# Kernel optimization log

Hardware: AMD Instinct MI355X
Metric: run time of the kernel (lower is better)

Reference implementation:

```python
import jax, jax.numpy as jnp
import numpy as np

B, T, V, E, DH, H, M, W = 64, 50, 32000, 64, 128, 8, 256, 50


def setup_inputs() -> dict:
    key = jax.random.key(0)
    ks = jax.random.split(key, 18)
    sc = 0.02
    return {
        "x": jax.random.randint(ks[0], (B, T), 0, V),
        "tok_emb": jax.random.normal(ks[1], (V, E)) * sc,
        "pos_emb": jax.random.normal(ks[2], (W, E)) * sc,
        "Wq": jax.random.normal(ks[3], (H, E, DH)) * sc,
        "bq": jnp.zeros((H, DH)),
        "Wk": jax.random.normal(ks[4], (H, E, DH)) * sc,
        "bk": jnp.zeros((H, DH)),
        "Wv": jax.random.normal(ks[5], (H, E, DH)) * sc,
        "bv": jnp.zeros((H, DH)),
        "Wo": jax.random.normal(ks[6], (H * DH, E)) * sc,
        "bo": jnp.zeros((E,)),
        "W1": jax.random.normal(ks[7], (E, M)) * sc,
        "b1": jnp.zeros((M,)),
        "W2": jax.random.normal(ks[8], (M, E)) * sc,
        "b2": jnp.zeros((E,)),
        "Wf": jax.random.normal(ks[9], (E, V)) * sc,
        "bf": jnp.zeros((V,)),
    }


def reference(x, tok_emb, pos_emb, Wq, bq, Wk, bk, Wv, bv, Wo, bo, W1, b1, W2, b2, Wf, bf):
    b, t = x.shape
    h = tok_emb[x] + pos_emb[:t]  # [B,T,E]
    # batched per-head QKV projections (original loops over 8 heads)
    Q = jnp.einsum("bte,hed->bhtd", h, Wq) + bq[None, :, None, :]
    K = jnp.einsum("bte,hed->bhtd", h, Wk) + bk[None, :, None, :]
    Vv = jnp.einsum("bte,hed->bhtd", h, Wv) + bv[None, :, None, :]
    scores = jnp.einsum("bhtd,bhsd->bhts", Q, K) / (DH ** 0.5)
    # faithful to original: masked_fill(tril(scores) == 0, -inf)
    scores = jnp.where(jnp.tril(scores) == 0, -jnp.inf, scores)
    attn = jax.nn.softmax(scores, axis=-1)
    o = jnp.einsum("bhts,bhsd->bhtd", attn, Vv)
    o = o.transpose(0, 2, 1, 3).reshape(b, t, H * DH)  # concat heads
    a = o @ Wo + bo
    # NOTE: no residual connections in the original module
    m = jax.nn.gelu(a @ W1 + b1, approximate=False)
    y = m @ W2 + b2
    logits = y @ Wf + bf  # [B,T,V]
    return logits
```

## Files before the change

kernel.cpp:

```cpp
#include <hip/hip_runtime.h>
#include <math.h>

#define T_ 50
#define R_ 3200

using u16 = unsigned short;
typedef __attribute__((ext_vector_type(8))) __bf16 bf16x8;
typedef __attribute__((ext_vector_type(4))) float f32x4;

__device__ __forceinline__ float bf2f(u16 u) {
  union { unsigned int i; float f; } x; x.i = ((unsigned int)u) << 16; return x.f;
}
__device__ __forceinline__ u16 f2bf(float f) {
  union { float f; unsigned int i; } x; x.f = f;
  unsigned int r = x.i + 0x7FFFu + ((x.i >> 16) & 1u);
  return (u16)(r >> 16);
}
__device__ __forceinline__ void split2(float v, u16& hi, u16& lo) {
  hi = f2bf(v);
  lo = f2bf(v - bf2f(hi));
}
__device__ __forceinline__ float gelu_f(float v) {
  return 0.5f * v * (1.0f + erff(v * 0.70710678118654752f));
}

__global__ __launch_bounds__(256) void k_prep(
    const int* __restrict__ x, const float* __restrict__ tok, const float* __restrict__ pos,
    const float* __restrict__ Wq, const float* __restrict__ Wk, const float* __restrict__ Wv,
    const float* __restrict__ bq, const float* __restrict__ bk, const float* __restrict__ bv,
    const float* __restrict__ Wo, const float* __restrict__ W1, const float* __restrict__ W2,
    const float* __restrict__ Wf,
    u16* __restrict__ hH, u16* __restrict__ hL,
    u16* __restrict__ WqkvTh, u16* __restrict__ WqkvTl, float* __restrict__ bqkv,
    u16* __restrict__ WoTh, u16* __restrict__ WoTl,
    u16* __restrict__ W1Th, u16* __restrict__ W1Tl,
    u16* __restrict__ W2Th, u16* __restrict__ W2Tl,
    u16* __restrict__ WfTh, u16* __restrict__ WfTl) {
  __shared__ __align__(16) float tile[64][68];
  int bid = blockIdx.x;
  if (bid < 800) {
    int i = bid * 256 + threadIdx.x;
    int row = i >> 6, e = i & 63;
    int t = row % T_;
    int v = x[row];
    split2(tok[(long)v * 64 + e] + pos[t * 64 + e], hH[i], hL[i]);
    return;
  }
  if (bid < 1964) {
    int i = (bid - 800) * 256 + threadIdx.x;
    const int S0 = 196608, S1 = 3072, S2 = 65536, S3 = 16384;
    if (i < S0) {
      int n = i >> 6, e = i & 63;
      int p = n >> 10, rem = n & 1023;
      int hh_ = rem >> 7, d = rem & 127;
      const float* W = (p == 0) ? Wq : ((p == 1) ? Wk : Wv);
      split2(W[hh_ * 8192 + e * 128 + d], WqkvTh[i], WqkvTl[i]);
      return;
    }
    i -= S0;
    if (i < S1) { int p = i >> 10, rem = i & 1023;
      const float* bb = (p == 0) ? bq : ((p == 1) ? bk : bv);
      bqkv[i] = bb[rem]; return; }
    i -= S1;
    if (i < S2) { int n = i >> 10, k = i & 1023;
      split2(Wo[k * 64 + n], WoTh[i], WoTl[i]); return; }
    i -= S2;
    if (i < S3) { int n = i >> 6, k = i & 63;
      split2(W1[k * 256 + n], W1Th[i], W1Tl[i]); return; }
    i -= S3;
    { int n = i >> 8, k = i & 255;
      split2(W2[k * 64 + n], W2Th[i], W2Tl[i]); }
    return;
  }
  int n0 = (bid - 1964) * 64;
  for (int c = threadIdx.x; c < 1024; c += 256) {
    int k = c >> 4, ch = (c & 15) * 4;
    *(float4*)&tile[k][ch] = *(const float4*)&Wf[(long)k * 32000 + n0 + ch];
  }
  __syncthreads();
  for (int c = threadIdx.x; c < 1024; c += 256) {
    int n = c >> 4, ch = (c & 15) * 4;
    u16 th[4], tl[4];
#pragma unroll
    for (int j = 0; j < 4; ++j) split2(tile[ch + j][n], th[j], tl[j]);
    *(ushort4*)&WfTh[(long)(n0 + n) * 64 + ch] = *(ushort4*)th;
    *(ushort4*)&WfTl[(long)(n0 + n) * 64 + ch] = *(ushort4*)tl;
  }
}

__global__ __launch_bounds__(256) void k_attn(const float* __restrict__ QKV,
                                              u16* __restrict__ Oh,
                                              u16* __restrict__ Ol) {
  __shared__ __align__(16) float Kl[64 * 128];
  __shared__ __align__(16) float Vt[128 * 64];
  __shared__ __align__(16) float Qw[4][512];
  __shared__ __align__(16) float Pw[4][256];
  const int bh = blockIdx.x, b = bh >> 3, hd = bh & 7;
  const int tid = threadIdx.x, lane = tid & 63, wave = tid >> 6;
  const float* base = QKV + (long)b * T_ * 3072 + hd * 128;
  for (int c = tid; c < 64 * 32; c += 256) {
    int s = c >> 5, c4 = c & 31;
    float4 kv = make_float4(0.f, 0.f, 0.f, 0.f), vv = kv;
    if (s < T_) {
      const float* rowp = base + (long)s * 3072;
      kv = *(const float4*)(rowp + 1024 + c4 * 4);
      vv = *(const float4*)(rowp + 2048 + c4 * 4);
    }
    *(float4*)&Kl[s * 128 + ((c4 ^ (s & 31)) << 2)] = kv;
    int d0 = c4 * 4, s4 = s >> 2, sm = s & 3;
    Vt[(d0 + 0) * 64 + ((s4 ^ ((d0 + 0) & 15)) << 2) + sm] = vv.x;
    Vt[(d0 + 1) * 64 + ((s4 ^ ((d0 + 1) & 15)) << 2) + sm] = vv.y;
    Vt[(d0 + 2) * 64 + ((s4 ^ ((d0 + 2) & 15)) << 2) + sm] = vv.z;
    Vt[(d0 + 3) * 64 + ((s4 ^ ((d0 + 3) & 15)) << 2) + sm] = vv.w;
  }
  __syncthreads();
  const float scale = 0.0883883476483184406f;
  for (int g = wave; g < 13; g += 4) {
    const int r0 = g * 4;
#pragma unroll
    for (int it = 0; it < 2; ++it) {
      int cc = lane + it * 64;
      int j = cc >> 5, c4q = cc & 31;
      int rq = r0 + j;
      if (rq < T_)
        *(float4*)&Qw[wave][j * 128 + c4q * 4] =
            *(const float4*)&base[(long)rq * 3072 + c4q * 4];
    }
    asm volatile("s_waitcnt lgkmcnt(0)" ::: "memory");
    float p0 = 0.f, p1 = 0.f, p2 = 0.f, p3 = 0.f;
#pragma unroll 8
    for (int c4 = 0; c4 < 32; ++c4) {
      float4 kv = *(const float4*)&Kl[lane * 128 + ((c4 ^ (lane & 31)) << 2)];
      float4 q0 = *(const float4*)&Qw[wave][c4 * 4];
      float4 q1 = *(const float4*)&Qw[wave][128 + c4 * 4];
      float4 q2 = *(const float4*)&Qw[wave][256 + c4 * 4];
      float4 q3 = *(const float4*)&Qw[wave][384 + c4 * 4];
      p0 = fmaf(q0.x, kv.x, p0); p0 = fmaf(q0.y, kv.y, p0);
      p0 = fmaf(q0.z, kv.z, p0); p0 = fmaf(q0.w, kv.w, p0);
      p1 = fmaf(q1.x, kv.x, p1); p1 = fmaf(q1.y, kv.y, p1);
      p1 = fmaf(q1.z, kv.z, p1); p1 = fmaf(q1.w, kv.w, p1);
      p2 = fmaf(q2.x, kv.x, p2); p2 = fmaf(q2.y, kv.y, p2);
      p2 = fmaf(q2.z, kv.z, p2); p2 = fmaf(q2.w, kv.w, p2);
      p3 = fmaf(q3.x, kv.x, p3); p3 = fmaf(q3.y, kv.y, p3);
      p3 = fmaf(q3.z, kv.z, p3); p3 = fmaf(q3.w, kv.w, p3);
    }
    float ps[4] = {p0, p1, p2, p3};
#pragma unroll
    for (int j = 0; j < 4; ++j) {
      int rq = r0 + j;
      float sc = (rq < T_ && lane <= rq) ? ps[j] * scale : -INFINITY;
      float mx = sc;
      mx = fmaxf(mx, __shfl_xor(mx, 32)); mx = fmaxf(mx, __shfl_xor(mx, 16));
      mx = fmaxf(mx, __shfl_xor(mx, 8));  mx = fmaxf(mx, __shfl_xor(mx, 4));
      mx = fmaxf(mx, __shfl_xor(mx, 2));  mx = fmaxf(mx, __shfl_xor(mx, 1));
      float e = expf(sc - mx);
      float sum = e;
      sum += __shfl_xor(sum, 32); sum += __shfl_xor(sum, 16); sum += __shfl_xor(sum, 8);
      sum += __shfl_xor(sum, 4);  sum += __shfl_xor(sum, 2);  sum += __shfl_xor(sum, 1);
      Pw[wave][j * 64 + lane] = e / sum;
    }
    asm volatile("s_waitcnt lgkmcnt(0)" ::: "memory");
    float oa[4] = {0.f, 0.f, 0.f, 0.f};
    float ob[4] = {0.f, 0.f, 0.f, 0.f};
    for (int s4 = 0; s4 <= g; ++s4) {
      int vc = (s4 ^ (lane & 15)) << 2;
      float4 va = *(const float4*)&Vt[lane * 64 + vc];
      float4 vb = *(const float4*)&Vt[(64 + lane) * 64 + vc];
#pragma unroll
      for (int j = 0; j < 4; ++j) {
        float4 pb = *(const float4*)&Pw[wave][j * 64 + s4 * 4];
        oa[j] = fmaf(pb.x, va.x, oa[j]); oa[j] = fmaf(pb.y, va.y, oa[j]);
        oa[j] = fmaf(pb.z, va.z, oa[j]); oa[j] = fmaf(pb.w, va.w, oa[j]);
        ob[j] = fmaf(pb.x, vb.x, ob[j]); ob[j] = fmaf(pb.y, vb.y, ob[j]);
        ob[j] = fmaf(pb.z, vb.z, ob[j]); ob[j] = fmaf(pb.w, vb.w, ob[j]);
      }
    }
#pragma unroll
    for (int j = 0; j < 4; ++j) {
      int rq = r0 + j;
      if (rq < T_) {
        long orow = ((long)b * T_ + rq) * 1024 + hd * 128;
        u16 hi, lo;
        split2(oa[j], hi, lo); Oh[orow + lane] = hi;      Ol[orow + lane] = lo;
        split2(ob[j], hi, lo); Oh[orow + 64 + lane] = hi; Ol[orow + 64 + lane] = lo;
      }
    }
  }
}

template <int WM, int TN, int KK, int ACT, int OSPLIT, int SWZ>
__global__ __launch_bounds__(WM * 64) void k_gemm(
    const u16* __restrict__ Ah, const u16* __restrict__ Al,
    const u16* __restrict__ Bth, const u16* __restrict__ Btl,
    const float* __restrict__ bias,
    float* __restrict__ C, u16* __restrict__ Ch, u16* __restrict__ Cl,
    int ldc, int gm) {
  int id = blockIdx.x;
  if constexpr (SWZ) {
    int nbk = gridDim.x;
    int q = nbk >> 3, r = nbk & 7;
    int xcd = id & 7, idx = id >> 3;
    id = (xcd < r ? xcd * (q + 1) : r * (q + 1) + (xcd - r) * q) + idx;
  }
  const int mb = id % gm, nb = id / gm;
  const int m0 = mb * (WM * 16), n0 = nb * (TN * 16);
  const int tid = threadIdx.x, lane = tid & 63, wave = tid >> 6;
  const int ln = lane & 15, quad = lane >> 4;
  const int mrow = m0 + wave * 16 + ln;
  const long arow = (long)mrow * KK;
  f32x4 acc[TN];
#pragma unroll
  for (int tn = 0; tn < TN; ++tn)
#pragma unroll
    for (int i = 0; i < 4; ++i) acc[tn][i] = 0.f;
#pragma unroll
  for (int k0 = 0; k0 < KK; k0 += 32) {
    bf16x8 a_h = *(const bf16x8*)&Ah[arow + k0 + quad * 8];
    bf16x8 a_l = *(const bf16x8*)&Al[arow + k0 + quad * 8];
#pragma unroll
    for (int tn = 0; tn < TN; ++tn) {
      const long brow = (long)(n0 + tn * 16 + ln) * KK + k0 + quad * 8;
      bf16x8 b_h = *(const bf16x8*)&Bth[brow];
      bf16x8 b_l = *(const bf16x8*)&Btl[brow];
      acc[tn] = __builtin_amdgcn_mfma_f32_16x16x32_bf16(b_h, a_h, acc[tn], 0, 0, 0);
      acc[tn] = __builtin_amdgcn_mfma_f32_16x16x32_bf16(b_h, a_l, acc[tn], 0, 0, 0);
      acc[tn] = __builtin_amdgcn_mfma_f32_16x16x32_bf16(b_l, a_h, acc[tn], 0, 0, 0);
    }
  }
#pragma unroll
  for (int tn = 0; tn < TN; ++tn) {
    int nc = n0 + tn * 16 + quad * 4;
    float4 bv = *(const float4*)&bias[nc];
    float v0 = acc[tn][0] + bv.x, v1 = acc[tn][1] + bv.y;
    float v2 = acc[tn][2] + bv.z, v3 = acc[tn][3] + bv.w;
    if (ACT) { v0 = gelu_f(v0); v1 = gelu_f(v1); v2 = gelu_f(v2); v3 = gelu_f(v3); }
    long idx2 = (long)mrow * ldc + nc;
    if constexpr (OSPLIT) {
      ushort4 hs, ls;
      split2(v0, hs.x, ls.x); split2(v1, hs.y, ls.y);
      split2(v2, hs.z, ls.z); split2(v3, hs.w, ls.w);
      *(ushort4*)&Ch[idx2] = hs;
      *(ushort4*)&Cl[idx2] = ls;
    } else {
      *(float4*)&C[idx2] = make_float4(v0, v1, v2, v3);
    }
  }
}

__global__ __launch_bounds__(64) void k_mlp(
    const u16* __restrict__ oH, const u16* __restrict__ oL,
    const u16* __restrict__ WoTh, const u16* __restrict__ WoTl, const float* __restrict__ bo,
    const u16* __restrict__ W1Th, const u16* __restrict__ W1Tl, const float* __restrict__ b1,
    const u16* __restrict__ W2Th, const u16* __restrict__ W2Tl, const float* __restrict__ b2,
    u16* __restrict__ yH, u16* __restrict__ yL) {
  __shared__ __align__(16) u16 aLh[16][88], aLl[16][88];
  __shared__ __align__(16) u16 mLh[16][264], mLl[16][264];
  const int lane = threadIdx.x, ln = lane & 15, quad = lane >> 4;
  const int r = blockIdx.x * 16 + ln;
  f32x4 acc1[4];
#pragma unroll
  for (int tn = 0; tn < 4; ++tn)
#pragma unroll
    for (int i = 0; i < 4; ++i) acc1[tn][i] = 0.f;
#pragma unroll 4
  for (int k0 = 0; k0 < 1024; k0 += 32) {
    bf16x8 a_h = *(const bf16x8*)&oH[(long)r * 1024 + k0 + quad * 8];
    bf16x8 a_l = *(const bf16x8*)&oL[(long)r * 1024 + k0 + quad * 8];
#pragma unroll
    for (int tn = 0; tn < 4; ++tn) {
      const int brow = (tn * 16 + ln) * 1024 + k0 + quad * 8;
      bf16x8 b_h = *(const bf16x8*)&WoTh[brow];
      bf16x8 b_l = *(const bf16x8*)&WoTl[brow];
      acc1[tn] = __builtin_amdgcn_mfma_f32_16x16x32_bf16(b_h, a_h, acc1[tn], 0, 0, 0);
      acc1[tn] = __builtin_amdgcn_mfma_f32_16x16x32_bf16(b_h, a_l, acc1[tn], 0, 0, 0);
      acc1[tn] = __builtin_amdgcn_mfma_f32_16x16x32_bf16(b_l, a_h, acc1[tn], 0, 0, 0);
    }
  }
#pragma unroll
  for (int tn = 0; tn < 4; ++tn) {
    int nc = tn * 16 + quad * 4;
    float4 bv = *(const float4*)&bo[nc];
    ushort4 hs, ls;
    split2(acc1[tn][0] + bv.x, hs.x, ls.x); split2(acc1[tn][1] + bv.y, hs.y, ls.y);
    split2(acc1[tn][2] + bv.z, hs.z, ls.z); split2(acc1[tn][3] + bv.w, hs.w, ls.w);
    *(ushort4*)&aLh[ln][nc] = hs;
    *(ushort4*)&aLl[ln][nc] = ls;
  }
  __syncthreads();
  f32x4 acc2[16];
#pragma unroll
  for (int tn = 0; tn < 16; ++tn)
#pragma unroll
    for (int i = 0; i < 4; ++i) acc2[tn][i] = 0.f;
#pragma unroll
  for (int k0 = 0; k0 < 64; k0 += 32) {
    bf16x8 a_h = *(const bf16x8*)&aLh[ln][k0 + quad * 8];
    bf16x8 a_l = *(const bf16x8*)&aLl[ln][k0 + quad * 8];
#pragma unroll
    for (int tn = 0; tn < 16; ++tn) {
      const int brow = (tn * 16 + ln) * 64 + k0 + quad * 8;
      bf16x8 b_h = *(const bf16x8*)&W1Th[brow];
      bf16x8 b_l = *(const bf16x8*)&W1Tl[brow];
      acc2[tn] = __builtin_amdgcn_mfma_f32_16x16x32_bf16(b_h, a_h, acc2[tn], 0, 0, 0);
      acc2[tn] = __builtin_amdgcn_mfma_f32_16x16x32_bf16(b_h, a_l, acc2[tn], 0, 0, 0);
      acc2[tn] = __builtin_amdgcn_mfma_f32_16x16x32_bf16(b_l, a_h, acc2[tn], 0, 0, 0);
    }
  }
#pragma unroll
  for (int tn = 0; tn < 16; ++tn) {
    int nc = tn * 16 + quad * 4;
    float4 bv = *(const float4*)&b1[nc];
    ushort4 hs, ls;
    split2(gelu_f(acc2[tn][0] + bv.x), hs.x, ls.x);
    split2(gelu_f(acc2[tn][1] + bv.y), hs.y, ls.y);
    split2(gelu_f(acc2[tn][2] + bv.z), hs.z, ls.z);
    split2(gelu_f(acc2[tn][3] + bv.w), hs.w, ls.w);
    *(ushort4*)&mLh[ln][nc] = hs;
    *(ushort4*)&mLl[ln][nc] = ls;
  }
  __syncthreads();
  f32x4 acc3[4];
#pragma unroll
  for (int tn = 0; tn < 4; ++tn)
#pragma unroll
    for (int i = 0; i < 4; ++i) acc3[tn][i] = 0.f;
#pragma unroll 2
  for (int k0 = 0; k0 < 256; k0 += 32) {
    bf16x8 a_h = *(const bf16x8*)&mLh[ln][k0 + quad * 8];
    bf16x8 a_l = *(const bf16x8*)&mLl[ln][k0 + quad * 8];
#pragma unroll
    for (int tn = 0; tn < 4; ++tn) {
      const int brow = (tn * 16 + ln) * 256 + k0 + quad * 8;
      bf16x8 b_h = *(const bf16x8*)&W2Th[brow];
      bf16x8 b_l = *(const bf16x8*)&W2Tl[brow];
      acc3[tn] = __builtin_amdgcn_mfma_f32_16x16x32_bf16(b_h, a_h, acc3[tn], 0, 0, 0);
      acc3[tn] = __builtin_amdgcn_mfma_f32_16x16x32_bf16(b_h, a_l, acc3[tn], 0, 0, 0);
      acc3[tn] = __builtin_amdgcn_mfma_f32_16x16x32_bf16(b_l, a_h, acc3[tn], 0, 0, 0);
    }
  }
#pragma unroll
  for (int tn = 0; tn < 4; ++tn) {
    int nc = tn * 16 + quad * 4;
    float4 bv = *(const float4*)&b2[nc];
    ushort4 hs, ls;
    split2(acc3[tn][0] + bv.x, hs.x, ls.x); split2(acc3[tn][1] + bv.y, hs.y, ls.y);
    split2(acc3[tn][2] + bv.z, hs.z, ls.z); split2(acc3[tn][3] + bv.w, hs.w, ls.w);
    *(ushort4*)&yH[(long)r * 64 + nc] = hs;
    *(ushort4*)&yL[(long)r * 64 + nc] = ls;
  }
}

extern "C" void kernel_launch(void* const* d_in, const int* in_sizes, int n_in,
                              void* d_out, int out_size, void* d_ws, size_t ws_size,
                              hipStream_t stream) {
  const int*   x   = (const int*)d_in[0];
  const float* tok = (const float*)d_in[1];
  const float* pos = (const float*)d_in[2];
  const float* Wq  = (const float*)d_in[3];
  const float* bq  = (const float*)d_in[4];
  const float* Wk  = (const float*)d_in[5];
  const float* bk  = (const float*)d_in[6];
  const float* Wv  = (const float*)d_in[7];
  const float* bv  = (const float*)d_in[8];
  const float* Wo  = (const float*)d_in[9];
  const float* bo  = (const float*)d_in[10];
  const float* W1  = (const float*)d_in[11];
  const float* b1  = (const float*)d_in[12];
  const float* W2  = (const float*)d_in[13];
  const float* b2  = (const float*)d_in[14];
  const float* Wf  = (const float*)d_in[15];
  const float* bfv = (const float*)d_in[16];

  char* ws = (char*)d_ws;
  float* QKV    = (float*)(ws + 0);
  u16*   oH     = (u16*)(ws + 39321600);
  u16*   oL     = (u16*)(ws + 45875200);
  u16*   hH     = (u16*)(ws + 52428800);
  u16*   hL     = (u16*)(ws + 52838400);
  u16*   yH     = (u16*)(ws + 53248000);
  u16*   yL     = (u16*)(ws + 53657600);
  u16*   WqkvTh = (u16*)(ws + 54067200);
  u16*   WqkvTl = (u16*)(ws + 54460416);
  float* bqkv   = (float*)(ws + 54853632);
  u16*   WoTh   = (u16*)(ws + 54865920);
  u16*   WoTl   = (u16*)(ws + 54996992);
  u16*   W1Th   = (u16*)(ws + 55128064);
  u16*   W1Tl   = (u16*)(ws + 55160832);
  u16*   W2Th   = (u16*)(ws + 55193600);
  u16*   W2Tl   = (u16*)(ws + 55226368);
  u16*   WfTh   = (u16*)(ws + 55259136);
  u16*   WfTl   = (u16*)(ws + 59355136);
  float* out    = (float*)d_out;

  k_prep<<<dim3(2464), 256, 0, stream>>>(x, tok, pos, Wq, Wk, Wv, bq, bk, bv,
      Wo, W1, W2, Wf, hH, hL, WqkvTh, WqkvTl, bqkv, WoTh, WoTl,
      W1Th, W1Tl, W2Th, W2Tl, WfTh, WfTl);
  k_gemm<4, 8, 64, 0, 0, 0><<<dim3(1200), 256, 0, stream>>>(
      hH, hL, WqkvTh, WqkvTl, bqkv, QKV, nullptr, nullptr, 3072, 50);
  k_attn<<<dim3(512), 256, 0, stream>>>(QKV, oH, oL);
  k_mlp<<<dim3(200), 64, 0, stream>>>(oH, oL, WoTh, WoTl, bo,
      W1Th, W1Tl, b1, W2Th, W2Tl, b2, yH, yL);
  k_gemm<4, 8, 64, 0, 0, 1><<<dim3(12500), 256, 0, stream>>>(
      yH, yL, WfTh, WfTl, bfv, out, nullptr, nullptr, 32000, 50);
}
```

Baseline: 732.9 us.

## Stage B tiles in LDS for GEMM and split fused MLP into GEMM launches

Result: faster. 602.7 us (-17.8%).

```diff
diff --git a/kernel.cpp b/kernel.cpp
--- a/kernel.cpp
+++ b/kernel.cpp
@@ -188,13 +188,18 @@
   }
 }
 
-template <int WM, int TN, int KK, int ACT, int OSPLIT, int SWZ>
-__global__ __launch_bounds__(WM * 64) void k_gemm(
+template <int BN, int BK, int ACT, int OSPLIT, int SWZ>
+__global__ __launch_bounds__(256) void k_gemm(
     const u16* __restrict__ Ah, const u16* __restrict__ Al,
     const u16* __restrict__ Bth, const u16* __restrict__ Btl,
     const float* __restrict__ bias,
     float* __restrict__ C, u16* __restrict__ Ch, u16* __restrict__ Cl,
-    int ldc, int gm) {
+    int ldc, int K, int gm) {
+  constexpr int BM = 64;
+  constexpr int TN = BN / 16;
+  constexpr int BKW = BK / 8;
+  __shared__ __align__(16) u16 Bh[BN][BK + 8];
+  __shared__ __align__(16) u16 Bl[BN][BK + 8];
   int id = blockIdx.x;
   if constexpr (SWZ) {
     int nbk = gridDim.x;
@@ -202,30 +207,40 @@
     int xcd = id & 7, idx = id >> 3;
     id = (xcd < r ? xcd * (q + 1) : r * (q + 1) + (xcd - r) * q) + idx;
   }
-  const int mb = id % gm, nb = id / gm;
-  const int m0 = mb * (WM * 16), n0 = nb * (TN * 16);
+  const int m0 = (id % gm) * BM, n0 = (id / gm) * BN;
   const int tid = threadIdx.x, lane = tid & 63, wave = tid >> 6;
   const int ln = lane & 15, quad = lane >> 4;
   const int mrow = m0 + wave * 16 + ln;
-  const long arow = (long)mrow * KK;
+  const long arow = (long)mrow * K;
   f32x4 acc[TN];
 #pragma unroll
   for (int tn = 0; tn < TN; ++tn)
 #pragma unroll
     for (int i = 0; i < 4; ++i) acc[tn][i] = 0.f;
-#pragma unroll
-  for (int k0 = 0; k0 < KK; k0 += 32) {
-    bf16x8 a_h = *(const bf16x8*)&Ah[arow + k0 + quad * 8];
-    bf16x8 a_l = *(const bf16x8*)&Al[arow + k0 + quad * 8];
-#pragma unroll
-    for (int tn = 0; tn < TN; ++tn) {
-      const long brow = (long)(n0 + tn * 16 + ln) * KK + k0 + quad * 8;
-      bf16x8 b_h = *(const bf16x8*)&Bth[brow];
-      bf16x8 b_l = *(const bf16x8*)&Btl[brow];
-      acc[tn] = __builtin_amdgcn_mfma_f32_16x16x32_bf16(b_h, a_h, acc[tn], 0, 0, 0);
-      acc[tn] = __builtin_amdgcn_mfma_f32_16x16x32_bf16(b_h, a_l, acc[tn], 0, 0, 0);
-      acc[tn] = __builtin_amdgcn_mfma_f32_16x16x32_bf16(b_l, a_h, acc[tn], 0, 0, 0);
-    }
+
+  for (int kk = 0; kk < K; kk += BK) {
+#pragma unroll
+    for (int c0 = 0; c0 < BN * BKW; c0 += 256) {
+      int c = c0 + tid;
+      int rr = c / BKW, c8 = (c % BKW) * 8;
+      *(uint4*)&Bh[rr][c8] = *(const uint4*)&Bth[(long)(n0 + rr) * K + kk + c8];
+      *(uint4*)&Bl[rr][c8] = *(const uint4*)&Btl[(long)(n0 + rr) * K + kk + c8];
+    }
+    __syncthreads();
+#pragma unroll
+    for (int ks = 0; ks < BK / 32; ++ks) {
+      bf16x8 a_h = *(const bf16x8*)&Ah[arow + kk + ks * 32 + quad * 8];
+      bf16x8 a_l = *(const bf16x8*)&Al[arow + kk + ks * 32 + quad * 8];
+#pragma unroll
+      for (int tn = 0; tn < TN; ++tn) {
+        bf16x8 b_h = *(const bf16x8*)&Bh[tn * 16 + ln][ks * 32 + quad * 8];
+        bf16x8 b_l = *(const bf16x8*)&Bl[tn * 16 + ln][ks * 32 + quad * 8];
+        acc[tn] = __builtin_amdgcn_mfma_f32_16x16x32_bf16(b_h, a_h, acc[tn], 0, 0, 0);
+        acc[tn] = __builtin_amdgcn_mfma_f32_16x16x32_bf16(b_h, a_l, acc[tn], 0, 0, 0);
+        acc[tn] = __builtin_amdgcn_mfma_f32_16x16x32_bf16(b_l, a_h, acc[tn], 0, 0, 0);
+      }
+    }
+    __syncthreads();
   }
 #pragma unroll
   for (int tn = 0; tn < TN; ++tn) {
@@ -244,109 +259,6 @@
     } else {
       *(float4*)&C[idx2] = make_float4(v0, v1, v2, v3);
     }
-  }
-}
-
-__global__ __launch_bounds__(64) void k_mlp(
-    const u16* __restrict__ oH, const u16* __restrict__ oL,
-    const u16* __restrict__ WoTh, const u16* __restrict__ WoTl, const float* __restrict__ bo,
-    const u16* __restrict__ W1Th, const u16* __restrict__ W1Tl, const float* __restrict__ b1,
-    const u16* __restrict__ W2Th, const u16* __restrict__ W2Tl, const float* __restrict__ b2,
-    u16* __restrict__ yH, u16* __restrict__ yL) {
-  __shared__ __align__(16) u16 aLh[16][88], aLl[16][88];
-  __shared__ __align__(16) u16 mLh[16][264], mLl[16][264];
-  const int lane = threadIdx.x, ln = lane & 15, quad = lane >> 4;
-  const int r = blockIdx.x * 16 + ln;
-  f32x4 acc1[4];
-#pragma unroll
-  for (int tn = 0; tn < 4; ++tn)
-#pragma unroll
-    for (int i = 0; i < 4; ++i) acc1[tn][i] = 0.f;
-#pragma unroll 4
-  for (int k0 = 0; k0 < 1024; k0 += 32) {
-    bf16x8 a_h = *(const bf16x8*)&oH[(long)r * 1024 + k0 + quad * 8];
-    bf16x8 a_l = *(const bf16x8*)&oL[(long)r * 1024 + k0 + quad * 8];
-#pragma unroll
-    for (int tn = 0; tn < 4; ++tn) {
-      const int brow = (tn * 16 + ln) * 1024 + k0 + quad * 8;
-      bf16x8 b_h = *(const bf16x8*)&WoTh[brow];
-      bf16x8 b_l = *(const bf16x8*)&WoTl[brow];
-      acc1[tn] = __builtin_amdgcn_mfma_f32_16x16x32_bf16(b_h, a_h, acc1[tn], 0, 0, 0);
-      acc1[tn] = __builtin_amdgcn_mfma_f32_16x16x32_bf16(b_h, a_l, acc1[tn], 0, 0, 0);
-      acc1[tn] = __builtin_amdgcn_mfma_f32_16x16x32_bf16(b_l, a_h, acc1[tn], 0, 0, 0);
-    }
-  }
-#pragma unroll
-  for (int tn = 0; tn < 4; ++tn) {
-    int nc = tn * 16 + quad * 4;
-    float4 bv = *(const float4*)&bo[nc];
-    ushort4 hs, ls;
-    split2(acc1[tn][0] + bv.x, hs.x, ls.x); split2(acc1[tn][1] + bv.y, hs.y, ls.y);
-    split2(acc1[tn][2] + bv.z, hs.z, ls.z); split2(acc1[tn][3] + bv.w, hs.w, ls.w);
-    *(ushort4*)&aLh[ln][nc] = hs;
-    *(ushort4*)&aLl[ln][nc] = ls;
-  }
-  __syncthreads();
-  f32x4 acc2[16];
-#pragma unroll
-  for (int tn = 0; tn < 16; ++tn)
-#pragma unroll
-    for (int i = 0; i < 4; ++i) acc2[tn][i] = 0.f;
-#pragma unroll
-  for (int k0 = 0; k0 < 64; k0 += 32) {
-    bf16x8 a_h = *(const bf16x8*)&aLh[ln][k0 + quad * 8];
-    bf16x8 a_l = *(const bf16x8*)&aLl[ln][k0 + quad * 8];
-#pragma unroll
-    for (int tn = 0; tn < 16; ++tn) {
-      const int brow = (tn * 16 + ln) * 64 + k0 + quad * 8;
-      bf16x8 b_h = *(const bf16x8*)&W1Th[brow];
-      bf16x8 b_l = *(const bf16x8*)&W1Tl[brow];
-      acc2[tn] = __builtin_amdgcn_mfma_f32_16x16x32_bf16(b_h, a_h, acc2[tn], 0, 0, 0);
-      acc2[tn] = __builtin_amdgcn_mfma_f32_16x16x32_bf16(b_h, a_l, acc2[tn], 0, 0, 0);
-      acc2[tn] = __builtin_amdgcn_mfma_f32_16x16x32_bf16(b_l, a_h, acc2[tn], 0, 0, 0);
-    }
-  }
-#pragma unroll
-  for (int tn = 0; tn < 16; ++tn) {
-    int nc = tn * 16 + quad * 4;
-    float4 bv = *(const float4*)&b1[nc];
-    ushort4 hs, ls;
-    split2(gelu_f(acc2[tn][0] + bv.x), hs.x, ls.x);
-    split2(gelu_f(acc2[tn][1] + bv.y), hs.y, ls.y);
-    split2(gelu_f(acc2[tn][2] + bv.z), hs.z, ls.z);
-    split2(gelu_f(acc2[tn][3] + bv.w), hs.w, ls.w);
-    *(ushort4*)&mLh[ln][nc] = hs;
-    *(ushort4*)&mLl[ln][nc] = ls;
-  }
-  __syncthreads();
-  f32x4 acc3[4];
-#pragma unroll
-  for (int tn = 0; tn < 4; ++tn)
-#pragma unroll
-    for (int i = 0; i < 4; ++i) acc3[tn][i] = 0.f;
-#pragma unroll 2
-  for (int k0 = 0; k0 < 256; k0 += 32) {
-    bf16x8 a_h = *(const bf16x8*)&mLh[ln][k0 + quad * 8];
-    bf16x8 a_l = *(const bf16x8*)&mLl[ln][k0 + quad * 8];
-#pragma unroll
-    for (int tn = 0; tn < 4; ++tn) {
-      const int brow = (tn * 16 + ln) * 256 + k0 + quad * 8;
-      bf16x8 b_h = *(const bf16x8*)&W2Th[brow];
-      bf16x8 b_l = *(const bf16x8*)&W2Tl[brow];
-      acc3[tn] = __builtin_amdgcn_mfma_f32_16x16x32_bf16(b_h, a_h, acc3[tn], 0, 0, 0);
-      acc3[tn] = __builtin_amdgcn_mfma_f32_16x16x32_bf16(b_h, a_l, acc3[tn], 0, 0, 0);
-      acc3[tn] = __builtin_amdgcn_mfma_f32_16x16x32_bf16(b_l, a_h, acc3[tn], 0, 0, 0);
-    }
-  }
-#pragma unroll
-  for (int tn = 0; tn < 4; ++tn) {
-    int nc = tn * 16 + quad * 4;
-    float4 bv = *(const float4*)&b2[nc];
-    ushort4 hs, ls;
-    split2(acc3[tn][0] + bv.x, hs.x, ls.x); split2(acc3[tn][1] + bv.y, hs.y, ls.y);
-    split2(acc3[tn][2] + bv.z, hs.z, ls.z); split2(acc3[tn][3] + bv.w, hs.w, ls.w);
-    *(ushort4*)&yH[(long)r * 64 + nc] = hs;
-    *(ushort4*)&yL[(long)r * 64 + nc] = ls;
   }
 }
 
@@ -377,29 +289,37 @@
   u16*   oL     = (u16*)(ws + 45875200);
   u16*   hH     = (u16*)(ws + 52428800);
   u16*   hL     = (u16*)(ws + 52838400);
-  u16*   yH     = (u16*)(ws + 53248000);
-  u16*   yL     = (u16*)(ws + 53657600);
-  u16*   WqkvTh = (u16*)(ws + 54067200);
-  u16*   WqkvTl = (u16*)(ws + 54460416);
-  float* bqkv   = (float*)(ws + 54853632);
-  u16*   WoTh   = (u16*)(ws + 54865920);
-  u16*   WoTl   = (u16*)(ws + 54996992);
-  u16*   W1Th   = (u16*)(ws + 55128064);
-  u16*   W1Tl   = (u16*)(ws + 55160832);
-  u16*   W2Th   = (u16*)(ws + 55193600);
-  u16*   W2Tl   = (u16*)(ws + 55226368);
-  u16*   WfTh   = (u16*)(ws + 55259136);
-  u16*   WfTl   = (u16*)(ws + 59355136);
+  u16*   aH     = (u16*)(ws + 53248000);
+  u16*   aL     = (u16*)(ws + 53657600);
+  u16*   mH     = (u16*)(ws + 54067200);
+  u16*   mL     = (u16*)(ws + 55705600);
+  u16*   yH     = (u16*)(ws + 57344000);
+  u16*   yL     = (u16*)(ws + 57753600);
+  u16*   WqkvTh = (u16*)(ws + 58163200);
+  u16*   WqkvTl = (u16*)(ws + 58556416);
+  float* bqkv   = (float*)(ws + 58949632);
+  u16*   WoTh   = (u16*)(ws + 58961920);
+  u16*   WoTl   = (u16*)(ws + 59092992);
+  u16*   W1Th   = (u16*)(ws + 59224064);
+  u16*   W1Tl   = (u16*)(ws + 59256832);
+  u16*   W2Th   = (u16*)(ws + 59289600);
+  u16*   W2Tl   = (u16*)(ws + 59322368);
+  u16*   WfTh   = (u16*)(ws + 59355136);
+  u16*   WfTl   = (u16*)(ws + 63451136);
   float* out    = (float*)d_out;
 
   k_prep<<<dim3(2464), 256, 0, stream>>>(x, tok, pos, Wq, Wk, Wv, bq, bk, bv,
       Wo, W1, W2, Wf, hH, hL, WqkvTh, WqkvTl, bqkv, WoTh, WoTl,
       W1Th, W1Tl, W2Th, W2Tl, WfTh, WfTl);
-  k_gemm<4, 8, 64, 0, 0, 0><<<dim3(1200), 256, 0, stream>>>(
-      hH, hL, WqkvTh, WqkvTl, bqkv, QKV, nullptr, nullptr, 3072, 50);
+  k_gemm<128, 64, 0, 0, 0><<<dim3(1200), 256, 0, stream>>>(
+      hH, hL, WqkvTh, WqkvTl, bqkv, QKV, nullptr, nullptr, 3072, 64, 50);
   k_attn<<<dim3(512), 256, 0, stream>>>(QKV, oH, oL);
-  k_mlp<<<dim3(200), 64, 0, stream>>>(oH, oL, WoTh, WoTl, bo,
-      W1Th, W1Tl, b1, W2Th, W2Tl, b2, yH, yL);
-  k_gemm<4, 8, 64, 0, 0, 1><<<dim3(12500), 256, 0, stream>>>(
-      yH, yL, WfTh, WfTl, bfv, out, nullptr, nullptr, 32000, 50);
-}
+  k_gemm<64, 256, 0, 1, 0><<<dim3(50), 256, 0, stream>>>(
+      oH, oL, WoTh, WoTl, bo, nullptr, aH, aL, 64, 1024, 50);
+  k_gemm<128, 64, 1, 1, 0><<<dim3(100), 256, 0, stream>>>(
+      aH, aL, W1Th, W1Tl, b1, nullptr, mH, mL, 256, 64, 50);
+  k_gemm<64, 256, 0, 1, 0><<<dim3(50), 256, 0, stream>>>(
+      mH, mL, W2Th, W2Tl, b2, nullptr, yH, yL, 64, 256, 50);
+  k_gemm<128, 64, 0, 0, 1><<<dim3(12500), 256, 0, stream>>>(
+      yH, yL, WfTh, WfTl, bfv, out, nullptr, nullptr, 32000, 64, 50);
+}
```
